# Performance work log

Measured on AMD Instinct MI355X. Metric: run time of the kernel, lower is better.

Reference implementation:

```python
import jax, jax.numpy as jnp
import numpy as np

MODEL_DIM = 1024
HEAD_DIM = 64
BATCH = 4
SEQ = 4096


def setup_inputs() -> dict:
    key = jax.random.key(0)
    ks = jax.random.split(key, 7)
    s = 1.0 / np.sqrt(MODEL_DIM)
    x = jax.random.normal(ks[0], (BATCH, SEQ, MODEL_DIM), dtype=jnp.float32)
    # causal lower-triangular boolean mask, broadcast over batch
    mask = jnp.tril(jnp.ones((SEQ, SEQ), dtype=jnp.bool_))
    Wk = jax.random.uniform(ks[1], (MODEL_DIM, HEAD_DIM), jnp.float32, -s, s)
    bk = jax.random.uniform(ks[2], (HEAD_DIM,), jnp.float32, -s, s)
    Wq = jax.random.uniform(ks[3], (MODEL_DIM, HEAD_DIM), jnp.float32, -s, s)
    bq = jax.random.uniform(ks[4], (HEAD_DIM,), jnp.float32, -s, s)
    Wv = jax.random.uniform(ks[5], (MODEL_DIM, HEAD_DIM), jnp.float32, -s, s)
    bv = jax.random.uniform(ks[6], (HEAD_DIM,), jnp.float32, -s, s)
    return {"x": x, "mask": mask, "Wk": Wk, "bk": bk, "Wq": Wq, "bq": bq, "Wv": Wv, "bv": bv}


def reference(x, mask, Wk, bk, Wq, bq, Wv, bv):
    # K, Q, V: (B, S, Dh)
    K = jnp.einsum('bsd,dh->bsh', x, Wk) + bk
    Q = jnp.einsum('bsd,dh->bsh', x, Wq) + bq
    V = jnp.einsum('bsd,dh->bsh', x, Wv) + bv
    scale = 1.0 / jnp.sqrt(jnp.asarray(HEAD_DIM, dtype=x.dtype))
    G = jnp.einsum('bqh,bkh->bqk', Q, K) * scale  # (B, S, S)
    G = jnp.where(mask[None, :, :], G, -jnp.inf)
    G = jax.nn.softmax(G, axis=-1)
    # dropout is identity at inference (eval mode)
    attn = jnp.einsum('bqk,bkh->bqh', G, V)
    return attn
```

## Files before the change

kernel.cpp:

```cpp
#include <hip/hip_runtime.h>
#include <hip/hip_bf16.h>
#include <stdint.h>

typedef __attribute__((ext_vector_type(8))) short bf16x8;
typedef __attribute__((ext_vector_type(4))) float f32x4;
typedef __attribute__((ext_vector_type(4))) unsigned short us4;

#define MFMA(a, b, c) __builtin_amdgcn_mfma_f32_16x16x32_bf16(a, b, c, 0, 0, 0)

__device__ __forceinline__ short f2bf(float f) {
    union { float f; uint32_t u; } v; v.f = f;
    uint32_t u = v.u;
    u = (u + 0x7FFFu + ((u >> 16) & 1u)) >> 16;
    return (short)u;
}

__global__ void wt_prep(const float* __restrict__ Wk, const float* __restrict__ bk,
                        const float* __restrict__ Wq, const float* __restrict__ bq,
                        const float* __restrict__ Wv, const float* __restrict__ bv,
                        short* __restrict__ WT, float* __restrict__ biasC) {
    int i = blockIdx.x * 256 + threadIdx.x;
    if (i < 192 * 1024) {
        int c = i >> 10, k = i & 1023, cc = c & 63;
        const float* W; float sc;
        if (c < 64)       { W = Wq; sc = 0.125f; }
        else if (c < 128) { W = Wk; sc = 1.0f;   }
        else              { W = Wv; sc = 1.0f;   }
        WT[i] = f2bf(W[k * 64 + cc] * sc);
    }
    if (blockIdx.x == 0 && threadIdx.x < 192) {
        int c = threadIdx.x;
        float bb;
        if (c < 64)       bb = bq[c] * 0.125f;
        else if (c < 128) bb = bk[c - 64];
        else              bb = bv[c - 128];
        biasC[c] = bb;
    }
}

__global__ __launch_bounds__(256) void qkv_proj(
        const float* __restrict__ X, const short* __restrict__ WT,
        const float* __restrict__ biasC,
        short* __restrict__ Qb, short* __restrict__ Kb, short* __restrict__ Vt) {
    const int lane = threadIdx.x & 63, w = threadIdx.x >> 6;
    const int row0 = blockIdx.x * 64;
    const int arow = row0 + w * 16 + (lane & 15);
    const int koff = (lane >> 4) * 8;

    f32x4 acc[12];
#pragma unroll
    for (int t = 0; t < 12; t++) acc[t] = (f32x4){0.f, 0.f, 0.f, 0.f};

    const float* xbase = X + (size_t)arow * 1024 + koff;
    const short* wbase = WT + (size_t)(lane & 15) * 1024 + koff;

    for (int kc = 0; kc < 1024; kc += 32) {
        const float4 a0 = *(const float4*)(xbase + kc);
        const float4 a1 = *(const float4*)(xbase + kc + 4);
        bf16x8 af;
        af[0] = f2bf(a0.x); af[1] = f2bf(a0.y); af[2] = f2bf(a0.z); af[3] = f2bf(a0.w);
        af[4] = f2bf(a1.x); af[5] = f2bf(a1.y); af[6] = f2bf(a1.z); af[7] = f2bf(a1.w);
#pragma unroll
        for (int ct = 0; ct < 12; ct++) {
            bf16x8 bf = *(const bf16x8*)(wbase + (size_t)ct * 16 * 1024 + kc);
            acc[ct] = MFMA(af, bf, acc[ct]);
        }
    }

    const int rbase = row0 + w * 16 + (lane >> 4) * 4;
    const int b = rbase >> 12, s0 = rbase & 4095;
#pragma unroll
    for (int ct = 0; ct < 12; ct++) {
        const int col = ct * 16 + (lane & 15);
        const float bias = biasC[col];
        if (ct < 4) {
            short* dst = Qb + (size_t)rbase * 64 + col;
#pragma unroll
            for (int r = 0; r < 4; r++) dst[r * 64] = f2bf(acc[ct][r] + bias);
        } else if (ct < 8) {
            short* dst = Kb + (size_t)rbase * 64 + (col - 64);
#pragma unroll
            for (int r = 0; r < 4; r++) dst[r * 64] = f2bf(acc[ct][r] + bias);
        } else {
            const int hd = col - 128;
            us4 pk;
#pragma unroll
            for (int r = 0; r < 4; r++) pk[r] = (unsigned short)f2bf(acc[ct][r] + bias);
            *(us4*)(Vt + ((size_t)(b * 64 + hd)) * 4096 + s0) = pk;
        }
    }
}

__global__ __launch_bounds__(256) void attn(
        const short* __restrict__ Qb, const short* __restrict__ Kb,
        const short* __restrict__ Vt, float* __restrict__ out) {
    const int lane = threadIdx.x & 63, w = threadIdx.x >> 6;
    const int bid = blockIdx.x;
    const int b = bid >> 8, qt = bid & 255;
    const int row16 = qt * 16;
    const int lt = qt >> 2;

    __shared__ short P_lds[4][16][64];
    __shared__ float c_m[4][16], c_l[4][16];
    __shared__ float c_o[4][16][64];

    const size_t bbase = (size_t)b * 4096 * 64;
    const int koff = (lane >> 4) * 8;

    const short* qp = Qb + bbase + (size_t)(row16 + (lane & 15)) * 64 + koff;
    const bf16x8 qf0 = *(const bf16x8*)(qp);
    const bf16x8 qf1 = *(const bf16x8*)(qp + 32);

    f32x4 o[4];
    float m[4], ls[4];
#pragma unroll
    for (int t = 0; t < 4; t++) { o[t] = (f32x4){0.f, 0.f, 0.f, 0.f}; m[t] = -__builtin_inff(); ls[t] = 0.f; }

    for (int kt = w; kt <= lt; kt += 4) {
        const short* kb = Kb + bbase + (size_t)kt * 64 * 64;
        f32x4 s[4];
#pragma unroll
        for (int c = 0; c < 4; c++) {
            const short* kp = kb + (size_t)(c * 16 + (lane & 15)) * 64 + koff;
            bf16x8 kf0 = *(const bf16x8*)(kp);
            bf16x8 kf1 = *(const bf16x8*)(kp + 32);
            f32x4 z = (f32x4){0.f, 0.f, 0.f, 0.f};
            z = MFMA(qf0, kf0, z);
            s[c] = MFMA(qf1, kf1, z);
        }
        if (kt == lt) {
#pragma unroll
            for (int c = 0; c < 4; c++) {
                const int key = kt * 64 + c * 16 + (lane & 15);
#pragma unroll
                for (int r = 0; r < 4; r++) {
                    const int q = row16 + (lane >> 4) * 4 + r;
                    if (key > q) s[c][r] = -1e30f;
                }
            }
        }
        float fac[4];
#pragma unroll
        for (int r = 0; r < 4; r++) {
            float v = fmaxf(fmaxf(s[0][r], s[1][r]), fmaxf(s[2][r], s[3][r]));
            v = fmaxf(v, __shfl_xor(v, 1));
            v = fmaxf(v, __shfl_xor(v, 2));
            v = fmaxf(v, __shfl_xor(v, 4));
            v = fmaxf(v, __shfl_xor(v, 8));
            const float mn = fmaxf(m[r], v);
            fac[r] = __expf(m[r] - mn);
            m[r] = mn;
        }
        f32x4 p[4];
#pragma unroll
        for (int c = 0; c < 4; c++)
#pragma unroll
            for (int r = 0; r < 4; r++)
                p[c][r] = __expf(s[c][r] - m[r]);
#pragma unroll
        for (int r = 0; r < 4; r++) {
            float rsv = p[0][r] + p[1][r] + p[2][r] + p[3][r];
            rsv += __shfl_xor(rsv, 1);
            rsv += __shfl_xor(rsv, 2);
            rsv += __shfl_xor(rsv, 4);
            rsv += __shfl_xor(rsv, 8);
            ls[r] = ls[r] * fac[r] + rsv;
        }
#pragma unroll
        for (int ct = 0; ct < 4; ct++)
#pragma unroll
            for (int r = 0; r < 4; r++) o[ct][r] *= fac[r];

#pragma unroll
        for (int c = 0; c < 4; c++)
#pragma unroll
            for (int r = 0; r < 4; r++)
                P_lds[w][(lane >> 4) * 4 + r][c * 16 + (lane & 15)] = f2bf(p[c][r]);

        bf16x8 pa0 = *(const bf16x8*)&P_lds[w][lane & 15][koff];
        bf16x8 pa1 = *(const bf16x8*)&P_lds[w][lane & 15][32 + koff];

        const short* vb = Vt + (size_t)b * 64 * 4096 + kt * 64;
#pragma unroll
        for (int ct = 0; ct < 4; ct++) {
            const short* vp = vb + (size_t)(ct * 16 + (lane & 15)) * 4096 + koff;
            bf16x8 vf0 = *(const bf16x8*)(vp);
            bf16x8 vf1 = *(const bf16x8*)(vp + 32);
            o[ct] = MFMA(pa0, vf0, o[ct]);
            o[ct] = MFMA(pa1, vf1, o[ct]);
        }
    }

    if ((lane & 15) == 0) {
#pragma unroll
        for (int r = 0; r < 4; r++) {
            c_m[w][(lane >> 4) * 4 + r] = m[r];
            c_l[w][(lane >> 4) * 4 + r] = ls[r];
        }
    }
#pragma unroll
    for (int ct = 0; ct < 4; ct++)
#pragma unroll
        for (int r = 0; r < 4; r++)
            c_o[w][(lane >> 4) * 4 + r][ct * 16 + (lane & 15)] = o[ct][r];
    __syncthreads();

    for (int idx = threadIdx.x; idx < 16 * 64; idx += 256) {
        const int row = idx >> 6, col = idx & 63;
        const float M = fmaxf(fmaxf(c_m[0][row], c_m[1][row]),
                              fmaxf(c_m[2][row], c_m[3][row]));
        float L = 0.f, val = 0.f;
#pragma unroll
        for (int ww = 0; ww < 4; ww++) {
            const float e = __expf(c_m[ww][row] - M);
            L += e * c_l[ww][row];
            val += e * c_o[ww][row][col];
        }
        out[bbase + (size_t)(row16 + row) * 64 + col] = val / L;
    }
}

extern "C" void kernel_launch(void* const* d_in, const int* in_sizes, int n_in,
                              void* d_out, int out_size, void* d_ws, size_t ws_size,
                              hipStream_t stream) {
    const float* x  = (const float*)d_in[0];
    const float* Wk = (const float*)d_in[2];
    const float* bk = (const float*)d_in[3];
    const float* Wq = (const float*)d_in[4];
    const float* bq = (const float*)d_in[5];
    const float* Wv = (const float*)d_in[6];
    const float* bv = (const float*)d_in[7];
    float* out = (float*)d_out;

    char* ws = (char*)d_ws;
    short* WT    = (short*)(ws);
    float* biasC = (float*)(ws + 393216);
    short* Qb    = (short*)(ws + (size_t)1 * (1 << 20));
    short* Kb    = (short*)(ws + (size_t)3 * (1 << 20));
    short* Vt    = (short*)(ws + (size_t)5 * (1 << 20));

    wt_prep<<<768, 256, 0, stream>>>(Wk, bk, Wq, bq, Wv, bv, WT, biasC);
    qkv_proj<<<256, 256, 0, stream>>>(x, WT, biasC, Qb, Kb, Vt);
    attn<<<1024, 256, 0, stream>>>(Qb, Kb, Vt, out);
}
```

Baseline: 149.4 us.

## Split-K QKV projection and transposed-S attention with 32-row tiles and exp2

The QKV projection now uses 16-row blocks with split-K across the four waves and an LDS reduction, launching 1024 blocks instead of 256 for better occupancy. Attention computes S transposed (K as the A operand), so P stays in registers and feeds a 16x16x16 MFMA directly, removing the LDS round trip for P. Each block handles 32 query rows in zig-zag order to balance the causal work, and the softmax folds log2(e) into the Q scale so it can use exp2. The trade-off is more registers per wave, an added reduction and sync in the projection, and reliance on inline asm for the bf16 pack.

```diff
diff --git a/kernel.cpp b/kernel.cpp
--- a/kernel.cpp
+++ b/kernel.cpp
@@ -3,10 +3,28 @@
 #include <stdint.h>
 
 typedef __attribute__((ext_vector_type(8))) short bf16x8;
+typedef __attribute__((ext_vector_type(4))) short bf16x4;
 typedef __attribute__((ext_vector_type(4))) float f32x4;
 typedef __attribute__((ext_vector_type(4))) unsigned short us4;
 
-#define MFMA(a, b, c) __builtin_amdgcn_mfma_f32_16x16x32_bf16(a, b, c, 0, 0, 0)
+#define MFMA32(a, b, c) __builtin_amdgcn_mfma_f32_16x16x32_bf16(a, b, c, 0, 0, 0)
+
+#if defined(__has_builtin) && __has_builtin(__builtin_amdgcn_mfma_f32_16x16x16bf16_1k)
+__device__ __forceinline__ f32x4 MFMA16(bf16x4 a, bf16x4 b, f32x4 c) {
+    return __builtin_amdgcn_mfma_f32_16x16x16bf16_1k(a, b, c, 0, 0, 0);
+}
+#elif defined(__has_builtin) && __has_builtin(__builtin_amdgcn_mfma_f32_16x16x16_bf16)
+__device__ __forceinline__ f32x4 MFMA16(bf16x4 a, bf16x4 b, f32x4 c) {
+    return __builtin_amdgcn_mfma_f32_16x16x16_bf16(a, b, c, 0, 0, 0);
+}
+#else
+__device__ __forceinline__ f32x4 MFMA16(bf16x4 a, bf16x4 b, f32x4 c) {
+    f32x4 d;
+    asm volatile("v_mfma_f32_16x16x16_bf16 %0, %1, %2, %3\n\ts_nop 7\n\ts_nop 2"
+                 : "=v"(d) : "v"(a), "v"(b), "v"(c));
+    return d;
+}
+#endif
 
 __device__ __forceinline__ short f2bf(float f) {
     union { float f; uint32_t u; } v; v.f = f;
@@ -14,6 +32,14 @@
     u = (u + 0x7FFFu + ((u >> 16) & 1u)) >> 16;
     return (short)u;
 }
+
+__device__ __forceinline__ uint32_t cvt_pk_bf16(float lo, float hi) {
+    uint32_t r;
+    asm("v_cvt_pk_bf16_f32 %0, %1, %2" : "=v"(r) : "v"(lo), "v"(hi));
+    return r;
+}
+
+#define QSCALE 0.18033688011112042f
 
 __global__ void wt_prep(const float* __restrict__ Wk, const float* __restrict__ bk,
                         const float* __restrict__ Wq, const float* __restrict__ bq,
@@ -23,7 +49,7 @@
     if (i < 192 * 1024) {
         int c = i >> 10, k = i & 1023, cc = c & 63;
         const float* W; float sc;
-        if (c < 64)       { W = Wq; sc = 0.125f; }
+        if (c < 64)       { W = Wq; sc = QSCALE; }
         else if (c < 128) { W = Wk; sc = 1.0f;   }
         else              { W = Wv; sc = 1.0f;   }
         WT[i] = f2bf(W[k * 64 + cc] * sc);
@@ -31,192 +57,205 @@
     if (blockIdx.x == 0 && threadIdx.x < 192) {
         int c = threadIdx.x;
         float bb;
-        if (c < 64)       bb = bq[c] * 0.125f;
+        if (c < 64)       bb = bq[c] * QSCALE;
         else if (c < 128) bb = bk[c - 64];
         else              bb = bv[c - 128];
         biasC[c] = bb;
     }
 }
 
-__global__ __launch_bounds__(256) void qkv_proj(
+__global__ __launch_bounds__(256, 4) void qkv_proj(
         const float* __restrict__ X, const short* __restrict__ WT,
         const float* __restrict__ biasC,
         short* __restrict__ Qb, short* __restrict__ Kb, short* __restrict__ Vt) {
     const int lane = threadIdx.x & 63, w = threadIdx.x >> 6;
-    const int row0 = blockIdx.x * 64;
-    const int arow = row0 + w * 16 + (lane & 15);
-    const int koff = (lane >> 4) * 8;
+    const int l15 = lane & 15, h = lane >> 4;
+    const int row0 = blockIdx.x * 16;
+    const int k0 = w * 256 + h * 8;
 
     f32x4 acc[12];
 #pragma unroll
     for (int t = 0; t < 12; t++) acc[t] = (f32x4){0.f, 0.f, 0.f, 0.f};
 
-    const float* xbase = X + (size_t)arow * 1024 + koff;
-    const short* wbase = WT + (size_t)(lane & 15) * 1024 + koff;
-
-    for (int kc = 0; kc < 1024; kc += 32) {
-        const float4 a0 = *(const float4*)(xbase + kc);
-        const float4 a1 = *(const float4*)(xbase + kc + 4);
+    const float* xb = X + (size_t)(row0 + l15) * 1024 + k0;
+    const short* wb = WT + (size_t)l15 * 1024 + k0;
+
+    for (int kc = 0; kc < 256; kc += 32) {
+        const float4 a0 = *(const float4*)(xb + kc);
+        const float4 a1 = *(const float4*)(xb + kc + 4);
         bf16x8 af;
         af[0] = f2bf(a0.x); af[1] = f2bf(a0.y); af[2] = f2bf(a0.z); af[3] = f2bf(a0.w);
         af[4] = f2bf(a1.x); af[5] = f2bf(a1.y); af[6] = f2bf(a1.z); af[7] = f2bf(a1.w);
 #pragma unroll
         for (int ct = 0; ct < 12; ct++) {
-            bf16x8 bf = *(const bf16x8*)(wbase + (size_t)ct * 16 * 1024 + kc);
-            acc[ct] = MFMA(af, bf, acc[ct]);
-        }
-    }
-
-    const int rbase = row0 + w * 16 + (lane >> 4) * 4;
-    const int b = rbase >> 12, s0 = rbase & 4095;
-#pragma unroll
-    for (int ct = 0; ct < 12; ct++) {
-        const int col = ct * 16 + (lane & 15);
-        const float bias = biasC[col];
-        if (ct < 4) {
-            short* dst = Qb + (size_t)rbase * 64 + col;
-#pragma unroll
-            for (int r = 0; r < 4; r++) dst[r * 64] = f2bf(acc[ct][r] + bias);
-        } else if (ct < 8) {
-            short* dst = Kb + (size_t)rbase * 64 + (col - 64);
-#pragma unroll
-            for (int r = 0; r < 4; r++) dst[r * 64] = f2bf(acc[ct][r] + bias);
-        } else {
-            const int hd = col - 128;
-            us4 pk;
-#pragma unroll
-            for (int r = 0; r < 4; r++) pk[r] = (unsigned short)f2bf(acc[ct][r] + bias);
-            *(us4*)(Vt + ((size_t)(b * 64 + hd)) * 4096 + s0) = pk;
-        }
-    }
-}
-
-__global__ __launch_bounds__(256) void attn(
+            bf16x8 bf = *(const bf16x8*)(wb + (size_t)ct * 16 * 1024 + kc);
+            acc[ct] = MFMA32(af, bf, acc[ct]);
+        }
+    }
+
+    __shared__ float buf[4][12][16][17];
+#pragma unroll
+    for (int ct = 0; ct < 12; ct++)
+#pragma unroll
+        for (int r = 0; r < 4; r++)
+            buf[w][ct][h * 4 + r][l15] = acc[ct][r];
+    __syncthreads();
+
+    const int b = row0 >> 12, srow = row0 & 4095;
+
+#pragma unroll
+    for (int i = 0; i < 8; i++) {
+        const int e = threadIdx.x + 256 * i;
+        const int ct = e >> 8, row = (e >> 4) & 15, col = e & 15;
+        float val = buf[0][ct][row][col] + buf[1][ct][row][col]
+                  + buf[2][ct][row][col] + buf[3][ct][row][col]
+                  + biasC[ct * 16 + col];
+        if (ct < 4) Qb[(size_t)(row0 + row) * 64 + ct * 16 + col] = f2bf(val);
+        else        Kb[(size_t)(row0 + row) * 64 + (ct - 4) * 16 + col] = f2bf(val);
+    }
+    {
+        const int ctv = (threadIdx.x >> 4) & 3;
+        const int col = threadIdx.x & 15;
+        const int rg = threadIdx.x >> 6;
+        const int hd = ctv * 16 + col;
+        const float bias = biasC[128 + hd];
+        us4 pk;
+#pragma unroll
+        for (int r = 0; r < 4; r++) {
+            const int row = rg * 4 + r;
+            float val = buf[0][8 + ctv][row][col] + buf[1][8 + ctv][row][col]
+                      + buf[2][8 + ctv][row][col] + buf[3][8 + ctv][row][col] + bias;
+            pk[r] = (unsigned short)f2bf(val);
+        }
+        *(us4*)(Vt + ((size_t)(b * 64 + hd)) * 4096 + srow + rg * 4) = pk;
+    }
+}
+
+__device__ __forceinline__ void softmax_update(const f32x4 s[4], float& m, float& l,
+                                               f32x4 o[4], bf16x4 pb[4]) {
+    float mx = s[0][0];
+#pragma unroll
+    for (int c = 0; c < 4; c++)
+#pragma unroll
+        for (int r = 0; r < 4; r++) mx = fmaxf(mx, s[c][r]);
+    mx = fmaxf(mx, __shfl_xor(mx, 16));
+    mx = fmaxf(mx, __shfl_xor(mx, 32));
+    const float mn = fmaxf(m, mx);
+    const float fac = exp2f(m - mn);
+    m = mn;
+    float p[4][4];
+    float sum = 0.f;
+#pragma unroll
+    for (int c = 0; c < 4; c++)
+#pragma unroll
+        for (int r = 0; r < 4; r++) { p[c][r] = exp2f(s[c][r] - mn); sum += p[c][r]; }
+    sum += __shfl_xor(sum, 16);
+    sum += __shfl_xor(sum, 32);
+    l = l * fac + sum;
+#pragma unroll
+    for (int c = 0; c < 4; c++) o[c] *= fac;
+#pragma unroll
+    for (int c = 0; c < 4; c++) {
+        union { bf16x4 v; uint32_t u[2]; } pk;
+        pk.u[0] = cvt_pk_bf16(p[c][0], p[c][1]);
+        pk.u[1] = cvt_pk_bf16(p[c][2], p[c][3]);
+        pb[c] = pk.v;
+    }
+}
+
+__global__ __launch_bounds__(256, 3) void attn(
         const short* __restrict__ Qb, const short* __restrict__ Kb,
         const short* __restrict__ Vt, float* __restrict__ out) {
-    const int lane = threadIdx.x & 63, w = threadIdx.x >> 6;
-    const int bid = blockIdx.x;
-    const int b = bid >> 8, qt = bid & 255;
-    const int row16 = qt * 16;
-    const int lt = qt >> 2;
-
-    __shared__ short P_lds[4][16][64];
-    __shared__ float c_m[4][16], c_l[4][16];
-    __shared__ float c_o[4][16][64];
-
+    const int lane = threadIdx.x & 63, wg = threadIdx.x >> 6;
+    const int l15 = lane & 15, h = lane >> 4;
+    const int g = blockIdx.x;
+    const int b = g >> 7;
+    const int i = g & 127;
+    const int u = (i & 1) ? (127 - (i >> 1)) : (i >> 1);
+    const int row32 = u * 32;
+    const int lt = u >> 1;
     const size_t bbase = (size_t)b * 4096 * 64;
-    const int koff = (lane >> 4) * 8;
-
-    const short* qp = Qb + bbase + (size_t)(row16 + (lane & 15)) * 64 + koff;
-    const bf16x8 qf0 = *(const bf16x8*)(qp);
-    const bf16x8 qf1 = *(const bf16x8*)(qp + 32);
-
-    f32x4 o[4];
-    float m[4], ls[4];
-#pragma unroll
-    for (int t = 0; t < 4; t++) { o[t] = (f32x4){0.f, 0.f, 0.f, 0.f}; m[t] = -__builtin_inff(); ls[t] = 0.f; }
-
-    for (int kt = w; kt <= lt; kt += 4) {
+
+    const short* qp0 = Qb + bbase + (size_t)(row32 + l15) * 64 + h * 8;
+    const short* qp1 = qp0 + 16 * 64;
+    const bf16x8 q00 = *(const bf16x8*)qp0,  q01 = *(const bf16x8*)(qp0 + 32);
+    const bf16x8 q10 = *(const bf16x8*)qp1,  q11 = *(const bf16x8*)(qp1 + 32);
+
+    f32x4 o0[4], o1[4];
+    float m0 = -__builtin_inff(), m1 = -__builtin_inff(), l0 = 0.f, l1 = 0.f;
+#pragma unroll
+    for (int t = 0; t < 4; t++) { o0[t] = (f32x4){0,0,0,0}; o1[t] = (f32x4){0,0,0,0}; }
+
+    for (int kt = wg; kt <= lt; kt += 4) {
         const short* kb = Kb + bbase + (size_t)kt * 64 * 64;
-        f32x4 s[4];
+        f32x4 s0[4], s1[4];
 #pragma unroll
         for (int c = 0; c < 4; c++) {
-            const short* kp = kb + (size_t)(c * 16 + (lane & 15)) * 64 + koff;
-            bf16x8 kf0 = *(const bf16x8*)(kp);
-            bf16x8 kf1 = *(const bf16x8*)(kp + 32);
-            f32x4 z = (f32x4){0.f, 0.f, 0.f, 0.f};
-            z = MFMA(qf0, kf0, z);
-            s[c] = MFMA(qf1, kf1, z);
+            const short* kp = kb + (size_t)(c * 16 + l15) * 64 + h * 8;
+            const bf16x8 kf0 = *(const bf16x8*)kp;
+            const bf16x8 kf1 = *(const bf16x8*)(kp + 32);
+            f32x4 z = (f32x4){0,0,0,0};
+            z = MFMA32(kf0, q00, z);  s0[c] = MFMA32(kf1, q01, z);
+            z = (f32x4){0,0,0,0};
+            z = MFMA32(kf0, q10, z);  s1[c] = MFMA32(kf1, q11, z);
         }
         if (kt == lt) {
+            const int q0g = row32 + l15, q1g = q0g + 16;
 #pragma unroll
             for (int c = 0; c < 4; c++) {
-                const int key = kt * 64 + c * 16 + (lane & 15);
 #pragma unroll
                 for (int r = 0; r < 4; r++) {
-                    const int q = row16 + (lane >> 4) * 4 + r;
-                    if (key > q) s[c][r] = -1e30f;
+                    const int key = kt * 64 + c * 16 + h * 4 + r;
+                    if (key > q0g) s0[c][r] = -1e30f;
+                    if (key > q1g) s1[c][r] = -1e30f;
                 }
             }
         }
-        float fac[4];
+        bf16x4 pb0[4], pb1[4];
+        softmax_update(s0, m0, l0, o0, pb0);
+        softmax_update(s1, m1, l1, o1, pb1);
+
+        const short* vb = Vt + (size_t)b * 64 * 4096 + kt * 64;
+#pragma unroll
+        for (int ct = 0; ct < 4; ct++) {
+            const short* vp = vb + (size_t)(ct * 16 + l15) * 4096 + h * 4;
+#pragma unroll
+            for (int c = 0; c < 4; c++) {
+                const bf16x4 vf = *(const bf16x4*)(vp + c * 16);
+                o0[ct] = MFMA16(vf, pb0[c], o0[ct]);
+                o1[ct] = MFMA16(vf, pb1[c], o1[ct]);
+            }
+        }
+    }
+
+    __shared__ float c_m[4][32], c_l[4][32];
+    __shared__ float c_o[4][64][33];
+    if (h == 0) {
+        c_m[wg][l15] = m0;  c_m[wg][16 + l15] = m1;
+        c_l[wg][l15] = l0;  c_l[wg][16 + l15] = l1;
+    }
+#pragma unroll
+    for (int ct = 0; ct < 4; ct++)
 #pragma unroll
         for (int r = 0; r < 4; r++) {
-            float v = fmaxf(fmaxf(s[0][r], s[1][r]), fmaxf(s[2][r], s[3][r]));
-            v = fmaxf(v, __shfl_xor(v, 1));
-            v = fmaxf(v, __shfl_xor(v, 2));
-            v = fmaxf(v, __shfl_xor(v, 4));
-            v = fmaxf(v, __shfl_xor(v, 8));
-            const float mn = fmaxf(m[r], v);
-            fac[r] = __expf(m[r] - mn);
-            m[r] = mn;
-        }
-        f32x4 p[4];
-#pragma unroll
-        for (int c = 0; c < 4; c++)
-#pragma unroll
-            for (int r = 0; r < 4; r++)
-                p[c][r] = __expf(s[c][r] - m[r]);
-#pragma unroll
-        for (int r = 0; r < 4; r++) {
-            float rsv = p[0][r] + p[1][r] + p[2][r] + p[3][r];
-            rsv += __shfl_xor(rsv, 1);
-            rsv += __shfl_xor(rsv, 2);
-            rsv += __shfl_xor(rsv, 4);
-            rsv += __shfl_xor(rsv, 8);
-            ls[r] = ls[r] * fac[r] + rsv;
-        }
-#pragma unroll
-        for (int ct = 0; ct < 4; ct++)
-#pragma unroll
-            for (int r = 0; r < 4; r++) o[ct][r] *= fac[r];
-
-#pragma unroll
-        for (int c = 0; c < 4; c++)
-#pragma unroll
-            for (int r = 0; r < 4; r++)
-                P_lds[w][(lane >> 4) * 4 + r][c * 16 + (lane & 15)] = f2bf(p[c][r]);
-
-        bf16x8 pa0 = *(const bf16x8*)&P_lds[w][lane & 15][koff];
-        bf16x8 pa1 = *(const bf16x8*)&P_lds[w][lane & 15][32 + koff];
-
-        const short* vb = Vt + (size_t)b * 64 * 4096 + kt * 64;
-#pragma unroll
-        for (int ct = 0; ct < 4; ct++) {
-            const short* vp = vb + (size_t)(ct * 16 + (lane & 15)) * 4096 + koff;
-            bf16x8 vf0 = *(const bf16x8*)(vp);
-            bf16x8 vf1 = *(const bf16x8*)(vp + 32);
-            o[ct] = MFMA(pa0, vf0, o[ct]);
-            o[ct] = MFMA(pa1, vf1, o[ct]);
-        }
-    }
-
-    if ((lane & 15) == 0) {
-#pragma unroll
-        for (int r = 0; r < 4; r++) {
-            c_m[w][(lane >> 4) * 4 + r] = m[r];
-            c_l[w][(lane >> 4) * 4 + r] = ls[r];
-        }
-    }
-#pragma unroll
-    for (int ct = 0; ct < 4; ct++)
-#pragma unroll
-        for (int r = 0; r < 4; r++)
-            c_o[w][(lane >> 4) * 4 + r][ct * 16 + (lane & 15)] = o[ct][r];
+            c_o[wg][ct * 16 + h * 4 + r][l15]      = o0[ct][r];
+            c_o[wg][ct * 16 + h * 4 + r][16 + l15] = o1[ct][r];
+        }
     __syncthreads();
 
-    for (int idx = threadIdx.x; idx < 16 * 64; idx += 256) {
-        const int row = idx >> 6, col = idx & 63;
-        const float M = fmaxf(fmaxf(c_m[0][row], c_m[1][row]),
-                              fmaxf(c_m[2][row], c_m[3][row]));
-        float L = 0.f, val = 0.f;
+#pragma unroll
+    for (int it = 0; it < 8; it++) {
+        const int e = threadIdx.x + 256 * it;
+        const int q = e >> 6, d = e & 63;
+        const float M = fmaxf(fmaxf(c_m[0][q], c_m[1][q]), fmaxf(c_m[2][q], c_m[3][q]));
+        float L = 0.f, V = 0.f;
 #pragma unroll
         for (int ww = 0; ww < 4; ww++) {
-            const float e = __expf(c_m[ww][row] - M);
-            L += e * c_l[ww][row];
-            val += e * c_o[ww][row][col];
-        }
-        out[bbase + (size_t)(row16 + row) * 64 + col] = val / L;
+            const float ee = exp2f(c_m[ww][q] - M);
+            L += ee * c_l[ww][q];
+            V += ee * c_o[ww][d][q];
+        }
+        out[bbase + (size_t)(row32 + q) * 64 + d] = V / L;
     }
 }
 
@@ -240,6 +279,6 @@
     short* Vt    = (short*)(ws + (size_t)5 * (1 << 20));
 
     wt_prep<<<768, 256, 0, stream>>>(Wk, bk, Wq, bq, Wv, bv, WT, biasC);
-    qkv_proj<<<256, 256, 0, stream>>>(x, WT, biasC, Qb, Kb, Vt);
-    attn<<<1024, 256, 0, stream>>>(Qb, Kb, Vt, out);
-}
+    qkv_proj<<<1024, 256, 0, stream>>>(x, WT, biasC, Qb, Kb, Vt);
+    attn<<<512, 256, 0, stream>>>(Qb, Kb, Vt, out);
+}
```

Measured after the change: 157.7 us. 5.5% more time.
